# Optimization experiments

Measured on AMD Instinct MI355X. Metric: run time of the kernel, lower is better.

## Reference

```python
import jax, jax.numpy as jnp
import numpy as np

RADIUS = [1.0, 1.5, 2.0, 100.0]  # bucket boundaries; last is catch-all
NFILT = len(RADIUS)
C_IN, C_OUT = 256, 512


def setup_inputs() -> dict:
    key = jax.random.key(0)
    k1, k2, k3, k4 = jax.random.split(key, 4)
    b, n = 16, 4096
    feat = jax.random.normal(k1, (b, n, C_IN), dtype=jnp.float32)
    xyz = jax.random.normal(k2, (b, n, 3), dtype=jnp.float32)
    # init per original reset_parameters
    std = 2.0 * np.sqrt(2.0 / (C_IN + C_OUT))
    a = np.sqrt(3.0) * std
    weight = jax.random.uniform(k3, (NFILT, C_OUT, C_IN), dtype=jnp.float32, minval=-a, maxval=a)
    bound = 1.0 / np.sqrt(C_IN)
    bias = jax.random.uniform(k4, (NFILT, C_OUT), dtype=jnp.float32, minval=-bound, maxval=bound)
    return {"feat": feat, "xyz": xyz, "weight": weight, "bias": bias}


def reference(feat, xyz, weight, bias):
    b, n, c = feat.shape
    p = feat.reshape(b * n, c)                      # (P, C)
    radii = jnp.asarray(RADIUS, dtype=feat.dtype)
    r_norm = jnp.linalg.norm(xyz.reshape(b * n, 3), axis=1)
    # first radius with r_norm < r (same as the sequential break in map2filtId)
    filt_id = jnp.argmax(r_norm[:, None] < radii[None, :], axis=1)  # (P,)
    # grouped linear expressed densely: all Nfilt GEMMs, then per-point select
    all_out = jnp.einsum('pc,foc->fpo', p, weight) + bias[:, None, :]  # (F, P, O)
    out = jnp.take_along_axis(all_out, filt_id[None, :, None], axis=0)[0]  # (P, O)
    return out.reshape(b, n, -1)
```

## Files before the change

kernel.cpp:

```cpp
#include <hip/hip_runtime.h>
#include <hip/hip_bf16.h>

#define C_IN   256
#define C_OUT  512
#define NFILT  4

#define BM 128
#define BN 128
#define BK 32
#define SAS 40

#define FBK 64

typedef __attribute__((ext_vector_type(8))) short bf16x8;
typedef __attribute__((ext_vector_type(4))) float floatx4;

union Pack8 { uint4 u; __hip_bfloat16 h[8]; };

__global__ void bucketize_kernel(const float* __restrict__ xyz,
                                 int* __restrict__ idxbuf,
                                 int* __restrict__ cnt, int P) {
    int pid = blockIdx.x * blockDim.x + threadIdx.x;
    if (pid >= P) return;
    float x = xyz[pid * 3 + 0];
    float y = xyz[pid * 3 + 1];
    float z = xyz[pid * 3 + 2];
    float r2 = __fadd_rn(__fadd_rn(__fmul_rn(x, x), __fmul_rn(y, y)), __fmul_rn(z, z));
    float r = sqrtf(r2);
    int filt;
    if (r < 1.0f)        filt = 0;
    else if (r < 1.5f)   filt = 1;
    else if (r < 2.0f)   filt = 2;
    else if (r < 100.0f) filt = 3;
    else                 filt = 0;

    int lane = threadIdx.x & 63;
    for (int f = 0; f < NFILT; ++f) {
        unsigned long long mask = __ballot(filt == f);
        if (mask == 0ull) continue;
        int leader = __ffsll((unsigned long long)mask) - 1;
        int base = 0;
        if (lane == leader) base = atomicAdd(&cnt[f], __popcll(mask));
        base = __shfl(base, leader);
        if (filt == f) {
            int off = __popcll(mask & ((1ull << lane) - 1ull));
            idxbuf[f * P + base + off] = pid;
        }
    }
}

__global__ void convert_w_kernel(const float* __restrict__ w,
                                 ushort* __restrict__ wb,
                                 int* __restrict__ cnt) {
    if (blockIdx.x == 0 && threadIdx.x < NFILT) cnt[threadIdx.x] = 0;
    int i = (blockIdx.x * blockDim.x + threadIdx.x) * 4;
    float4 v = *(const float4*)(w + i);
    union { ushort4 u; __hip_bfloat16 h[4]; } cv;
    cv.h[0] = __float2bfloat16(v.x);
    cv.h[1] = __float2bfloat16(v.y);
    cv.h[2] = __float2bfloat16(v.z);
    cv.h[3] = __float2bfloat16(v.w);
    *(ushort4*)(wb + i) = cv.u;
}

__global__ __launch_bounds__(256) void gather_kernel(
    const float* __restrict__ feat, const int* __restrict__ idxbuf,
    const int* __restrict__ cnt, ushort* __restrict__ gA, int P)
{
    int wid = threadIdx.x >> 6;
    int lane = threadIdx.x & 63;
    int slot = blockIdx.x * 4 + wid;
    if (slot >= P) return;
    int c0 = cnt[0], c1 = cnt[1], c2 = cnt[2];
    int b1 = c0, b2 = c0 + c1, b3 = c0 + c1 + c2;
    int f, i;
    if (slot < b1)      { f = 0; i = slot; }
    else if (slot < b2) { f = 1; i = slot - b1; }
    else if (slot < b3) { f = 2; i = slot - b2; }
    else                { f = 3; i = slot - b3; }
    int pid = idxbuf[f * P + i];
    float4 v = *(const float4*)(feat + (size_t)pid * C_IN + lane * 4);
    union { ushort4 u; __hip_bfloat16 h[4]; } cv;
    cv.h[0] = __float2bfloat16(v.x);
    cv.h[1] = __float2bfloat16(v.y);
    cv.h[2] = __float2bfloat16(v.z);
    cv.h[3] = __float2bfloat16(v.w);
    *(ushort4*)(gA + (size_t)slot * C_IN + lane * 4) = cv.u;
}

__global__ __launch_bounds__(256) void gemm_fast_kernel(
    const ushort* __restrict__ gA, const ushort* __restrict__ wb,
    const float* __restrict__ bias, const int* __restrict__ idxbuf,
    const int* __restrict__ cnt, float* __restrict__ out, int P)
{
    __shared__ ushort sA[BM * FBK];
    __shared__ ushort sB[BN * FBK];
    __shared__ int    sIdx[BM];
    __shared__ float  sBias[BN];

    int lid = blockIdx.x + (blockIdx.y << 2);
    int g = lid & 7;
    int q = lid >> 3;
    int cTile = q & 3;
    int t = ((q >> 2) << 3) + g;

    int c0 = cnt[0], c1 = cnt[1], c2 = cnt[2], c3 = cnt[3];
    int counts[4] = {c0, c1, c2, c3};
    int bases[4]  = {0, c0, c0 + c1, c0 + c1 + c2};
    int f = -1, lt = 0;
    for (int ff = 0; ff < 4; ++ff) {
        int nt = (counts[ff] + BM - 1) / BM;
        if (t < nt) { f = ff; lt = t; break; }
        t -= nt;
    }
    if (f < 0) return;

    int tid = threadIdx.x;
    int oBase = cTile * BN;
    int cn = counts[f];
    int gBase = bases[f] + lt * BM;
    int wRow0 = f * C_OUT + oBase;

    if (tid < BM) {
        int r = lt * BM + tid;
        sIdx[tid] = (r < cn) ? idxbuf[f * P + r] : -1;
    }
    if (tid < BN) sBias[tid] = bias[f * C_OUT + oBase + tid];
    __syncthreads();

    int wid = tid >> 6;
    int lane = tid & 63;
    int wm = (wid >> 1) * 64;
    int wn = (wid & 1) * 64;
    int lcol = lane & 15;
    int quad = lane >> 4;
    int rp = lcol & 7;

    int lrow = lane >> 3;
    int lchunk = lane & 7;
    int schunk = lchunk ^ lrow;

    floatx4 acc[4][4];
#pragma unroll
    for (int i = 0; i < 4; ++i)
#pragma unroll
        for (int j = 0; j < 4; ++j)
            acc[i][j] = (floatx4){0.f, 0.f, 0.f, 0.f};

    const char* aBase = (const char*)gA;
    const char* bBase = (const char*)wb;

#pragma unroll
    for (int s = 0; s < C_IN / FBK; ++s) {
        int kByte = s * (FBK * 2);
#pragma unroll
        for (int n = 0; n < 4; ++n) {
            int seg = wid * 4 + n;
            int row = seg * 8 + lrow;
            const char* srcA = aBase + ((size_t)(gBase + row) * (C_IN * 2)) + kByte + schunk * 16;
            __builtin_amdgcn_global_load_lds(
                (const __attribute__((address_space(1))) void*)srcA,
                (__attribute__((address_space(3))) void*)&sA[seg * 512], 16, 0, 0);
            const char* srcB = bBase + ((size_t)(wRow0 + row) * (C_IN * 2)) + kByte + schunk * 16;
            __builtin_amdgcn_global_load_lds(
                (const __attribute__((address_space(1))) void*)srcB,
                (__attribute__((address_space(3))) void*)&sB[seg * 512], 16, 0, 0);
        }
        asm volatile("s_waitcnt vmcnt(0)" ::: "memory");
        __builtin_amdgcn_s_barrier();
        __builtin_amdgcn_sched_barrier(0);

#pragma unroll
        for (int kk2 = 0; kk2 < 2; ++kk2) {
            int ck = ((kk2 * 4 + quad) ^ rp) * 8;
            bf16x8 af[4], bfr[4];
#pragma unroll
            for (int i = 0; i < 4; ++i)
                af[i] = *(const bf16x8*)&sA[(wm + i * 16 + lcol) * FBK + ck];
#pragma unroll
            for (int j = 0; j < 4; ++j)
                bfr[j] = *(const bf16x8*)&sB[(wn + j * 16 + lcol) * FBK + ck];
#pragma unroll
            for (int i = 0; i < 4; ++i)
#pragma unroll
                for (int j = 0; j < 4; ++j)
                    acc[i][j] = __builtin_amdgcn_mfma_f32_16x16x32_bf16(af[i], bfr[j], acc[i][j], 0, 0, 0);
        }
        if (s < C_IN / FBK - 1) __syncthreads();
    }

#pragma unroll
    for (int i = 0; i < 4; ++i) {
        int r0 = wm + i * 16 + quad * 4;
        int pid0 = sIdx[r0 + 0];
        int pid1 = sIdx[r0 + 1];
        int pid2 = sIdx[r0 + 2];
        int pid3 = sIdx[r0 + 3];
#pragma unroll
        for (int j = 0; j < 4; ++j) {
            int o = oBase + wn + j * 16 + lcol;
            float bv = sBias[wn + j * 16 + lcol];
            if (pid0 >= 0) out[pid0 * C_OUT + o] = acc[i][j][0] + bv;
            if (pid1 >= 0) out[pid1 * C_OUT + o] = acc[i][j][1] + bv;
            if (pid2 >= 0) out[pid2 * C_OUT + o] = acc[i][j][2] + bv;
            if (pid3 >= 0) out[pid3 * C_OUT + o] = acc[i][j][3] + bv;
        }
    }
}

__global__ __launch_bounds__(256) void gemm_kernel(
    const float* __restrict__ feat, const ushort* __restrict__ wb,
    const float* __restrict__ bias, const int* __restrict__ idxbuf,
    const int* __restrict__ cnt, float* __restrict__ out, int P)
{
    __shared__ ushort sA[BM * SAS];
    __shared__ ushort sB[BN * SAS];
    __shared__ int    sIdx[BM];
    __shared__ float  sBias[BN];

    int lid = blockIdx.x + (blockIdx.y << 2);
    int g = lid & 7;
    int q = lid >> 3;
    int cTile = q & 3;
    int t = ((q >> 2) << 3) + g;

    int counts[4];
    counts[0] = cnt[0]; counts[1] = cnt[1]; counts[2] = cnt[2]; counts[3] = cnt[3];
    int f = -1, lt = 0;
    for (int ff = 0; ff < 4; ++ff) {
        int nt = (counts[ff] + BM - 1) / BM;
        if (t < nt) { f = ff; lt = t; break; }
        t -= nt;
    }
    if (f < 0) return;

    int tid = threadIdx.x;
    int oBase = cTile * BN;
    int rowBase = lt * BM;
    int cn = counts[f];

    if (tid < BM) {
        int r = rowBase + tid;
        sIdx[tid] = (r < cn) ? idxbuf[f * P + r] : -1;
    }
    if (tid < BN) sBias[tid] = bias[f * C_OUT + oBase + tid];
    __syncthreads();

    int sRow = tid >> 1;
    int sHalf = tid & 1;
    int myIdx = sIdx[sRow];
    const float* aRow = feat + (size_t)(myIdx < 0 ? 0 : myIdx) * C_IN + sHalf * 16;
    const ushort* bRow = wb + (size_t)(f * C_OUT + oBase + sRow) * C_IN + sHalf * 16;

    int wid = tid >> 6;
    int lane = tid & 63;
    int wm = (wid >> 1) * 64;
    int wn = (wid & 1) * 64;
    int lcol = lane & 15;
    int quad = lane >> 4;

    floatx4 acc[4][4];
#pragma unroll
    for (int i = 0; i < 4; ++i)
#pragma unroll
        for (int j = 0; j < 4; ++j)
            acc[i][j] = (floatx4){0.f, 0.f, 0.f, 0.f};

    for (int kk = 0; kk < C_IN; kk += BK) {
        const float* ap = aRow + kk;
        float4 a0 = *(const float4*)(ap + 0);
        float4 a1 = *(const float4*)(ap + 4);
        float4 a2 = *(const float4*)(ap + 8);
        float4 a3 = *(const float4*)(ap + 12);
        const ushort* bp = bRow + kk;
        uint4 b01 = *(const uint4*)(bp + 0);
        uint4 b23 = *(const uint4*)(bp + 8);

        Pack8 p0, p1;
        p0.h[0] = __float2bfloat16(a0.x); p0.h[1] = __float2bfloat16(a0.y);
        p0.h[2] = __float2bfloat16(a0.z); p0.h[3] = __float2bfloat16(a0.w);
        p0.h[4] = __float2bfloat16(a1.x); p0.h[5] = __float2bfloat16(a1.y);
        p0.h[6] = __float2bfloat16(a1.z); p0.h[7] = __float2bfloat16(a1.w);
        p1.h[0] = __float2bfloat16(a2.x); p1.h[1] = __float2bfloat16(a2.y);
        p1.h[2] = __float2bfloat16(a2.z); p1.h[3] = __float2bfloat16(a2.w);
        p1.h[4] = __float2bfloat16(a3.x); p1.h[5] = __float2bfloat16(a3.y);
        p1.h[6] = __float2bfloat16(a3.z); p1.h[7] = __float2bfloat16(a3.w);

        ushort* dA = &sA[sRow * SAS + sHalf * 16];
        *(uint4*)(dA + 0) = p0.u;
        *(uint4*)(dA + 8) = p1.u;
        ushort* dB = &sB[sRow * SAS + sHalf * 16];
        *(uint4*)(dB + 0) = b01;
        *(uint4*)(dB + 8) = b23;

        __syncthreads();

        bf16x8 af[4], bfr[4];
#pragma unroll
        for (int i = 0; i < 4; ++i)
            af[i] = *(const bf16x8*)&sA[(wm + i * 16 + lcol) * SAS + quad * 8];
#pragma unroll
        for (int j = 0; j < 4; ++j)
            bfr[j] = *(const bf16x8*)&sB[(wn + j * 16 + lcol) * SAS + quad * 8];
#pragma unroll
        for (int i = 0; i < 4; ++i)
#pragma unroll
            for (int j = 0; j < 4; ++j)
                acc[i][j] = __builtin_amdgcn_mfma_f32_16x16x32_bf16(af[i], bfr[j], acc[i][j], 0, 0, 0);

        __syncthreads();
    }

#pragma unroll
    for (int i = 0; i < 4; ++i) {
        int r0 = wm + i * 16 + quad * 4;
        int pid0 = sIdx[r0 + 0];
        int pid1 = sIdx[r0 + 1];
        int pid2 = sIdx[r0 + 2];
        int pid3 = sIdx[r0 + 3];
#pragma unroll
        for (int j = 0; j < 4; ++j) {
            int o = oBase + wn + j * 16 + lcol;
            float bv = sBias[wn + j * 16 + lcol];
            if (pid0 >= 0) out[pid0 * C_OUT + o] = acc[i][j][0] + bv;
            if (pid1 >= 0) out[pid1 * C_OUT + o] = acc[i][j][1] + bv;
            if (pid2 >= 0) out[pid2 * C_OUT + o] = acc[i][j][2] + bv;
            if (pid3 >= 0) out[pid3 * C_OUT + o] = acc[i][j][3] + bv;
        }
    }
}

extern "C" void kernel_launch(void* const* d_in, const int* in_sizes, int n_in,
                              void* d_out, int out_size, void* d_ws, size_t ws_size,
                              hipStream_t stream) {
    const float* feat = (const float*)d_in[0];
    const float* xyz  = (const float*)d_in[1];
    const float* w    = (const float*)d_in[2];
    const float* bias = (const float*)d_in[3];
    float* out = (float*)d_out;
    int P = in_sizes[0] / C_IN;

    char* ws = (char*)d_ws;
    size_t offIdx = 0;
    size_t offCnt = (size_t)4 * P * 4;
    size_t offWb  = offCnt + 16;
    size_t offGA  = (offWb + (size_t)NFILT * C_OUT * C_IN * 2 + 255) & ~(size_t)255;
    size_t needed = offGA + (size_t)(P + BM) * C_IN * 2;

    int* idxbuf = (int*)(ws + offIdx);
    int* cntp   = (int*)(ws + offCnt);
    ushort* wb  = (ushort*)(ws + offWb);

    convert_w_kernel<<<(NFILT * C_OUT * C_IN) / 1024, 256, 0, stream>>>(w, wb, cntp);
    bucketize_kernel<<<(P + 255) / 256, 256, 0, stream>>>(xyz, idxbuf, cntp, P);

    int tilesY = ((P / BM + NFILT + 7) / 8) * 8;
    dim3 grid(C_OUT / BN, tilesY);

    if (ws_size >= needed) {
        ushort* gA = (ushort*)(ws + offGA);
        gather_kernel<<<(P + 3) / 4, 256, 0, stream>>>(feat, idxbuf, cntp, gA, P);
        gemm_fast_kernel<<<grid, 256, 0, stream>>>(gA, wb, bias, idxbuf, cntp, out, P);
    } else {
        gemm_kernel<<<grid, 256, 0, stream>>>(feat, wb, bias, idxbuf, cntp, out, P);
    }
}
```

Baseline: 278.4 us.

## Double-buffer GEMM LDS tiles and aggregate bucketize atomics per block

```diff
diff --git a/kernel.cpp b/kernel.cpp
--- a/kernel.cpp
+++ b/kernel.cpp
@@ -17,36 +17,48 @@
 
 union Pack8 { uint4 u; __hip_bfloat16 h[8]; };
 
-__global__ void bucketize_kernel(const float* __restrict__ xyz,
-                                 int* __restrict__ idxbuf,
-                                 int* __restrict__ cnt, int P) {
-    int pid = blockIdx.x * blockDim.x + threadIdx.x;
-    if (pid >= P) return;
-    float x = xyz[pid * 3 + 0];
-    float y = xyz[pid * 3 + 1];
-    float z = xyz[pid * 3 + 2];
-    float r2 = __fadd_rn(__fadd_rn(__fmul_rn(x, x), __fmul_rn(y, y)), __fmul_rn(z, z));
-    float r = sqrtf(r2);
-    int filt;
-    if (r < 1.0f)        filt = 0;
-    else if (r < 1.5f)   filt = 1;
-    else if (r < 2.0f)   filt = 2;
-    else if (r < 100.0f) filt = 3;
-    else                 filt = 0;
-
-    int lane = threadIdx.x & 63;
+__global__ __launch_bounds__(1024) void bucketize_kernel(
+    const float* __restrict__ xyz, int* __restrict__ idxbuf,
+    int* __restrict__ cnt, int P)
+{
+    __shared__ int hist[NFILT];
+    __shared__ int wbase[16][NFILT];
+    __shared__ int gbase[NFILT];
+
+    int tid = threadIdx.x;
+    int wid = tid >> 6;
+    int lane = tid & 63;
+    if (tid < NFILT) hist[tid] = 0;
+    __syncthreads();
+
+    int pid = blockIdx.x * 1024 + tid;
+    int filt = -1;
+    if (pid < P) {
+        float x = xyz[pid * 3 + 0];
+        float y = xyz[pid * 3 + 1];
+        float z = xyz[pid * 3 + 2];
+        float r2 = __fadd_rn(__fadd_rn(__fmul_rn(x, x), __fmul_rn(y, y)), __fmul_rn(z, z));
+        float r = sqrtf(r2);
+        if (r < 1.0f)        filt = 0;
+        else if (r < 1.5f)   filt = 1;
+        else if (r < 2.0f)   filt = 2;
+        else if (r < 100.0f) filt = 3;
+        else                 filt = 0;
+    }
+
+    int myoff = 0;
+#pragma unroll
     for (int f = 0; f < NFILT; ++f) {
-        unsigned long long mask = __ballot(filt == f);
-        if (mask == 0ull) continue;
-        int leader = __ffsll((unsigned long long)mask) - 1;
-        int base = 0;
-        if (lane == leader) base = atomicAdd(&cnt[f], __popcll(mask));
-        base = __shfl(base, leader);
-        if (filt == f) {
-            int off = __popcll(mask & ((1ull << lane) - 1ull));
-            idxbuf[f * P + base + off] = pid;
-        }
-    }
+        unsigned long long m = __ballot(filt == f);
+        if (lane == 0) wbase[wid][f] = atomicAdd(&hist[f], (int)__popcll(m));
+        if (filt == f) myoff = __popcll(m & ((1ull << lane) - 1ull));
+    }
+    __syncthreads();
+    if (tid < NFILT) gbase[tid] = atomicAdd(&cnt[tid], hist[tid]);
+    __syncthreads();
+
+    if (filt >= 0)
+        idxbuf[filt * P + gbase[filt] + wbase[wid][filt] + myoff] = pid;
 }
 
 __global__ void convert_w_kernel(const float* __restrict__ w,
@@ -88,13 +100,32 @@
     *(ushort4*)(gA + (size_t)slot * C_IN + lane * 4) = cv.u;
 }
 
+#define STAGE(s, b) do {                                                        \
+    int kByte = (s) * (FBK * 2);                                                \
+    _Pragma("unroll")                                                           \
+    for (int n = 0; n < 4; ++n) {                                               \
+        int seg = wid * 4 + n;                                                  \
+        int row = seg * 8 + lrow;                                               \
+        const char* srcA = aBase + ((size_t)(gBase + row) * (C_IN * 2))         \
+                                 + kByte + schunk * 16;                         \
+        __builtin_amdgcn_global_load_lds(                                       \
+            (const __attribute__((address_space(1))) void*)srcA,                \
+            (__attribute__((address_space(3))) void*)&sA[b][seg * 512], 16, 0, 0); \
+        const char* srcB = bBase + ((size_t)(wRow0 + row) * (C_IN * 2))         \
+                                 + kByte + schunk * 16;                         \
+        __builtin_amdgcn_global_load_lds(                                       \
+            (const __attribute__((address_space(1))) void*)srcB,                \
+            (__attribute__((address_space(3))) void*)&sB[b][seg * 512], 16, 0, 0); \
+    }                                                                           \
+} while (0)
+
 __global__ __launch_bounds__(256) void gemm_fast_kernel(
     const ushort* __restrict__ gA, const ushort* __restrict__ wb,
     const float* __restrict__ bias, const int* __restrict__ idxbuf,
     const int* __restrict__ cnt, float* __restrict__ out, int P)
 {
-    __shared__ ushort sA[BM * FBK];
-    __shared__ ushort sB[BN * FBK];
+    __shared__ ushort sA[2][BM * FBK];
+    __shared__ ushort sB[2][BN * FBK];
     __shared__ int    sIdx[BM];
     __shared__ float  sBias[BN];
 
@@ -121,13 +152,6 @@
     int gBase = bases[f] + lt * BM;
     int wRow0 = f * C_OUT + oBase;
 
-    if (tid < BM) {
-        int r = lt * BM + tid;
-        sIdx[tid] = (r < cn) ? idxbuf[f * P + r] : -1;
-    }
-    if (tid < BN) sBias[tid] = bias[f * C_OUT + oBase + tid];
-    __syncthreads();
-
     int wid = tid >> 6;
     int lane = tid & 63;
     int wm = (wid >> 1) * 64;
@@ -140,6 +164,17 @@
     int lchunk = lane & 7;
     int schunk = lchunk ^ lrow;
 
+    const char* aBase = (const char*)gA;
+    const char* bBase = (const char*)wb;
+
+    STAGE(0, 0);
+    if (tid < BM) {
+        int r = lt * BM + tid;
+        sIdx[tid] = (r < cn) ? idxbuf[f * P + r] : -1;
+    }
+    if (tid < BN) sBias[tid] = bias[f * C_OUT + oBase + tid];
+    __syncthreads();
+
     floatx4 acc[4][4];
 #pragma unroll
     for (int i = 0; i < 4; ++i)
@@ -147,46 +182,32 @@
         for (int j = 0; j < 4; ++j)
             acc[i][j] = (floatx4){0.f, 0.f, 0.f, 0.f};
 
-    const char* aBase = (const char*)gA;
-    const char* bBase = (const char*)wb;
-
 #pragma unroll
     for (int s = 0; s < C_IN / FBK; ++s) {
-        int kByte = s * (FBK * 2);
-#pragma unroll
-        for (int n = 0; n < 4; ++n) {
-            int seg = wid * 4 + n;
-            int row = seg * 8 + lrow;
-            const char* srcA = aBase + ((size_t)(gBase + row) * (C_IN * 2)) + kByte + schunk * 16;
-            __builtin_amdgcn_global_load_lds(
-                (const __attribute__((address_space(1))) void*)srcA,
-                (__attribute__((address_space(3))) void*)&sA[seg * 512], 16, 0, 0);
-            const char* srcB = bBase + ((size_t)(wRow0 + row) * (C_IN * 2)) + kByte + schunk * 16;
-            __builtin_amdgcn_global_load_lds(
-                (const __attribute__((address_space(1))) void*)srcB,
-                (__attribute__((address_space(3))) void*)&sB[seg * 512], 16, 0, 0);
+        if (s < C_IN / FBK - 1) STAGE(s + 1, (s + 1) & 1);
+
+        const ushort* cA = sA[s & 1];
+        const ushort* cB = sB[s & 1];
+#pragma unroll
+        for (int kk2 = 0; kk2 < 2; ++kk2) {
+            int ck = ((kk2 * 4 + quad) ^ rp) * 8;
+            bf16x8 af[4], bfr[4];
+#pragma unroll
+            for (int i = 0; i < 4; ++i)
+                af[i] = *(const bf16x8*)&cA[(wm + i * 16 + lcol) * FBK + ck];
+#pragma unroll
+            for (int j = 0; j < 4; ++j)
+                bfr[j] = *(const bf16x8*)&cB[(wn + j * 16 + lcol) * FBK + ck];
+#pragma unroll
+            for (int i = 0; i < 4; ++i)
+#pragma unroll
+                for (int j = 0; j < 4; ++j)
+                    acc[i][j] = __builtin_amdgcn_mfma_f32_16x16x32_bf16(af[i], bfr[j], acc[i][j], 0, 0, 0);
         }
+
         asm volatile("s_waitcnt vmcnt(0)" ::: "memory");
         __builtin_amdgcn_s_barrier();
         __builtin_amdgcn_sched_barrier(0);
-
-#pragma unroll
-        for (int kk2 = 0; kk2 < 2; ++kk2) {
-            int ck = ((kk2 * 4 + quad) ^ rp) * 8;
-            bf16x8 af[4], bfr[4];
-#pragma unroll
-            for (int i = 0; i < 4; ++i)
-                af[i] = *(const bf16x8*)&sA[(wm + i * 16 + lcol) * FBK + ck];
-#pragma unroll
-            for (int j = 0; j < 4; ++j)
-                bfr[j] = *(const bf16x8*)&sB[(wn + j * 16 + lcol) * FBK + ck];
-#pragma unroll
-            for (int i = 0; i < 4; ++i)
-#pragma unroll
-                for (int j = 0; j < 4; ++j)
-                    acc[i][j] = __builtin_amdgcn_mfma_f32_16x16x32_bf16(af[i], bfr[j], acc[i][j], 0, 0, 0);
-        }
-        if (s < C_IN / FBK - 1) __syncthreads();
     }
 
 #pragma unroll
@@ -352,7 +373,7 @@
     ushort* wb  = (ushort*)(ws + offWb);
 
     convert_w_kernel<<<(NFILT * C_OUT * C_IN) / 1024, 256, 0, stream>>>(w, wb, cntp);
-    bucketize_kernel<<<(P + 255) / 256, 256, 0, stream>>>(xyz, idxbuf, cntp, P);
+    bucketize_kernel<<<(P + 1023) / 1024, 1024, 0, stream>>>(xyz, idxbuf, cntp, P);
 
     int tilesY = ((P / BM + NFILT + 7) / 8) * 8;
     dim3 grid(C_OUT / BN, tilesY);
```

After: 233.8 us. 16.0% less time.
